# Performance work log

Measured on AMD Instinct MI355X. Metric: run time of the kernel, lower is better.

The kernel has to match this reference:

```python
import jax, jax.numpy as jnp
import numpy as np

N, F, H, O = 3072, 128, 16, 8  # nodes, in_channels, hidden_channels, out_channels


def setup_inputs() -> dict:
    key = jax.random.key(0)
    ks = jax.random.split(key, 8)
    s = 0.01  # xavier gain=0.01 in original init -> small weights
    return {
        "x": jax.random.normal(ks[0], (N, F), dtype=jnp.float32),
        "edge_index": jax.random.randint(ks[1], (2, N * 32), 0, N, dtype=jnp.int64),
        "node_distances": jax.random.uniform(ks[2], (N, N), dtype=jnp.float32),
        "normalization_matrix": jnp.ones((N, N), dtype=jnp.float32),
        # per-feature MLPs fs[f]: Linear(1,H) -> ReLU -> (Dropout p=0) -> Linear(H,O), stacked over F
        "W1": s * jax.random.normal(ks[3], (F, H), dtype=jnp.float32),
        "b1": jnp.zeros((F, H), dtype=jnp.float32),
        "W2": s * jax.random.normal(ks[4], (F, H, O), dtype=jnp.float32),
        "b2": jnp.zeros((F, O), dtype=jnp.float32),
        # rho MLP: Linear(1,H) -> ReLU -> Linear(H,O) (bias=True since is_graph_task=False)
        "rW1": s * jax.random.normal(ks[5], (H,), dtype=jnp.float32),
        "rb1": jnp.zeros((H,), dtype=jnp.float32),
        "rW2": s * jax.random.normal(ks[6], (H, O), dtype=jnp.float32),
        "rb2": jnp.zeros((O,), dtype=jnp.float32),
    }


def reference(x, edge_index, node_distances, normalization_matrix,
              W1, b1, W2, b2, rW1, rb1, rW2, rb2):
    # --- per-feature tiny MLPs, vectorized over the feature axis ---
    # h[n,f,:] = relu(x[n,f] * W1[f] + b1[f])
    h = jax.nn.relu(x[:, :, None] * W1[None, :, :] + b1[None, :, :])  # [N,F,H]
    fx = jnp.einsum('nfh,fho->nfo', h, W2) + b2[None, :, :]           # [N,F,O]
    # sum over features first (commutes with the matmul's F-reduction)
    g = fx.sum(axis=1)                                                 # [N,O]

    # --- rho MLP on normalized pairwise distances ---
    d = node_distances / normalization_matrix                          # [N,N]
    hd = jax.nn.relu(d[:, :, None] * rW1 + rb1)                        # [N,N,H]
    m = jnp.einsum('nmh,ho->nmo', hd, rW2) + rb2                       # [N,N,O]

    # out.T in torch: mf = m_dist_perm @ fx_perm summed over features -> [N,O]
    out = jnp.einsum('nmo,mo->no', m, g)                               # [N,O]
    return out
```

## Files before the change

### kernel.cpp

```cpp
#include <hip/hip_runtime.h>
#include <hip/hip_bf16.h>
#include <math.h>

#define NN 3072
#define FF 128
#define HH 16
#define OO 8

#define OFF_GT   0

#define NPB 4

__global__ __launch_bounds__(128) void gnan_g_kernel(
    const float* __restrict__ x,
    const float* __restrict__ W1,
    const float* __restrict__ b1,
    const float* __restrict__ W2,
    const float* __restrict__ b2,
    float* __restrict__ gT)
{
    const int f  = threadIdx.x;
    const int n0 = blockIdx.x * NPB;

    float xv[NPB];
#pragma unroll
    for (int ni = 0; ni < NPB; ++ni)
        xv[ni] = x[(size_t)(n0 + ni) * FF + f];

    const float4 b2a = *reinterpret_cast<const float4*>(b2 + f * OO);
    const float4 b2b = *reinterpret_cast<const float4*>(b2 + f * OO + 4);

    float acc[NPB][OO];
#pragma unroll
    for (int ni = 0; ni < NPB; ++ni) {
        acc[ni][0] = b2a.x; acc[ni][1] = b2a.y; acc[ni][2] = b2a.z; acc[ni][3] = b2a.w;
        acc[ni][4] = b2b.x; acc[ni][5] = b2b.y; acc[ni][6] = b2b.z; acc[ni][7] = b2b.w;
    }

    for (int h = 0; h < HH; ++h) {
        const float w1h = W1[f * HH + h];
        const float b1h = b1[f * HH + h];
        const float4 wa = *reinterpret_cast<const float4*>(W2 + (size_t)(f * HH + h) * OO);
        const float4 wb = *reinterpret_cast<const float4*>(W2 + (size_t)(f * HH + h) * OO + 4);
#pragma unroll
        for (int ni = 0; ni < NPB; ++ni) {
            const float a = fmaxf(fmaf(xv[ni], w1h, b1h), 0.f);
            acc[ni][0] = fmaf(a, wa.x, acc[ni][0]);
            acc[ni][1] = fmaf(a, wa.y, acc[ni][1]);
            acc[ni][2] = fmaf(a, wa.z, acc[ni][2]);
            acc[ni][3] = fmaf(a, wa.w, acc[ni][3]);
            acc[ni][4] = fmaf(a, wb.x, acc[ni][4]);
            acc[ni][5] = fmaf(a, wb.y, acc[ni][5]);
            acc[ni][6] = fmaf(a, wb.z, acc[ni][6]);
            acc[ni][7] = fmaf(a, wb.w, acc[ni][7]);
        }
    }

    __shared__ float wsum[NPB][2][OO];
    const int lane = threadIdx.x & 63;
    const int wid  = threadIdx.x >> 6;
#pragma unroll
    for (int ni = 0; ni < NPB; ++ni) {
#pragma unroll
        for (int o = 0; o < OO; ++o) {
#pragma unroll
            for (int off = 32; off > 0; off >>= 1)
                acc[ni][o] += __shfl_down(acc[ni][o], off);
        }
        if (lane == 0) {
#pragma unroll
            for (int o = 0; o < OO; ++o) wsum[ni][wid][o] = acc[ni][o];
        }
    }
    __syncthreads();
    if (threadIdx.x < NPB * OO) {
        const int ni = threadIdx.x >> 3, o = threadIdx.x & 7;
        gT[o * NN + (n0 + ni)] = wsum[ni][0][o] + wsum[ni][1][o];
    }
}

__device__ __forceinline__ void accum_one(
    float d, float clo, float chi, const float gk[OO],
    float dg[OO], float sg[OO], float corr[OO],
    const float* KpS, const float (*rowsS)[16], const float* refB)
{
#pragma unroll
    for (int o = 0; o < OO; ++o) sg[o] += gk[o];
    if (d >= clo && d < chi) {
#pragma unroll
        for (int o = 0; o < OO; ++o) dg[o] = fmaf(d, gk[o], dg[o]);
    } else {
        int j = 0;
#pragma unroll
        for (int p = 0; p < HH; ++p) j += (d >= KpS[1 + p]) ? 1 : 0;
#pragma unroll
        for (int o = 0; o < OO; ++o) {
            const float v = fmaf(rowsS[j][o], d, rowsS[j][8 + o]) - refB[o];
            corr[o] = fmaf(v, gk[o], corr[o]);
        }
    }
}

__global__ __launch_bounds__(256) void gnan_main_kernel(
    const float* __restrict__ nd,
    const float* __restrict__ nm,
    const float* __restrict__ gT,
    const float* __restrict__ rW1,
    const float* __restrict__ rb1,
    const float* __restrict__ rW2,
    const float* __restrict__ rb2,
    float* __restrict__ out)
{
    __shared__ float KpS[HH + 2];
    __shared__ float rowsS[HH + 1][16];
    __shared__ float refS[18];

    const int t = threadIdx.x;

    if (t < (HH + 1) * OO + 2) {
        float w[HH], bb[HH], knee[HH];
#pragma unroll
        for (int h = 0; h < HH; ++h) {
            w[h]  = rW1[h];
            bb[h] = rb1[h];
            knee[h] = (w[h] != 0.f) ? (-bb[h] / w[h]) : INFINITY;
        }
        if (t >= (HH + 1) * OO) {
            KpS[(t - (HH + 1) * OO) * (HH + 1)] =
                (t == (HH + 1) * OO) ? -INFINITY : INFINITY;
        } else {
            const int j = t >> 3, o = t & 7;
            if (o == 0 && j < HH) {
                int r = 0;
#pragma unroll
                for (int h2 = 0; h2 < HH; ++h2)
                    r += (knee[h2] < knee[j] || (knee[h2] == knee[j] && h2 < j)) ? 1 : 0;
                KpS[1 + r] = knee[j];
            }
            float cAdd = rb2[o];
#pragma unroll
            for (int h = 0; h < HH; ++h)
                if (w[h] == 0.f) cAdd += fmaxf(bb[h], 0.f) * rW2[h * OO + o];

            float alpha = 0.f, beta = 0.f;
#pragma unroll
            for (int h = 0; h < HH; ++h) {
                int r = 0;
#pragma unroll
                for (int h2 = 0; h2 < HH; ++h2)
                    r += (knee[h2] < knee[h] || (knee[h2] == knee[h] && h2 < h)) ? 1 : 0;
                const bool active = (w[h] > 0.f) ? (r < j)
                                  : (w[h] < 0.f ? (r >= j) : false);
                if (active) {
                    alpha += w[h]  * rW2[h * OO + o];
                    beta  += bb[h] * rW2[h * OO + o];
                }
            }
            const float betaF = beta + cAdd;
            rowsS[j][o]     = alpha;
            rowsS[j][8 + o] = betaF;

            const float d00 = nd[0] / nm[0];
            int j0 = 0;
#pragma unroll
            for (int h = 0; h < HH; ++h) j0 += (d00 >= knee[h]) ? 1 : 0;
            if (j == j0) {
                refS[2 + o]  = alpha;
                refS[10 + o] = betaF;
                if (o == 0) {
                    float clo = -INFINITY, chi = INFINITY;
#pragma unroll
                    for (int h = 0; h < HH; ++h) {
                        if (d00 >= knee[h]) clo = fmaxf(clo, knee[h]);
                        else                chi = fminf(chi, knee[h]);
                    }
                    refS[0] = clo;
                    refS[1] = chi;
                }
            }
        }
    }
    __syncthreads();

    const int wave = t >> 6;
    const int lane = t & 63;
    const int row  = blockIdx.x * 4 + wave;

    const float clo = refS[0];
    const float chi = refS[1];
    const float* refB = &refS[10];

    const float* __restrict__ drow = nd + (size_t)row * NN;
    const float* __restrict__ nrow = nm + (size_t)row * NN;

    float dg[OO], sg[OO], corr[OO];
#pragma unroll
    for (int o = 0; o < OO; ++o) { dg[o] = 0.f; sg[o] = 0.f; corr[o] = 0.f; }

    for (int it = 0; it < NN / 256; ++it) {
        const int m0 = it * 256 + lane * 4;
        const float4 dv = *reinterpret_cast<const float4*>(drow + m0);
        const float4 nv = *reinterpret_cast<const float4*>(nrow + m0);
        float4 gv[OO];
#pragma unroll
        for (int o = 0; o < OO; ++o)
            gv[o] = *reinterpret_cast<const float4*>(&gT[o * NN + m0]);

        {
            float gk[OO];
#pragma unroll
            for (int o = 0; o < OO; ++o) gk[o] = gv[o].x;
            accum_one(__fdividef(dv.x, nv.x), clo, chi, gk, dg, sg, corr, KpS, rowsS, refB);
        }
        {
            float gk[OO];
#pragma unroll
            for (int o = 0; o < OO; ++o) gk[o] = gv[o].y;
            accum_one(__fdividef(dv.y, nv.y), clo, chi, gk, dg, sg, corr, KpS, rowsS, refB);
        }
        {
            float gk[OO];
#pragma unroll
            for (int o = 0; o < OO; ++o) gk[o] = gv[o].z;
            accum_one(__fdividef(dv.z, nv.z), clo, chi, gk, dg, sg, corr, KpS, rowsS, refB);
        }
        {
            float gk[OO];
#pragma unroll
            for (int o = 0; o < OO; ++o) gk[o] = gv[o].w;
            accum_one(__fdividef(dv.w, nv.w), clo, chi, gk, dg, sg, corr, KpS, rowsS, refB);
        }
    }

    float val[OO];
#pragma unroll
    for (int o = 0; o < OO; ++o)
        val[o] = fmaf(refS[2 + o], dg[o], fmaf(refB[o], sg[o], corr[o]));
#pragma unroll
    for (int o = 0; o < OO; ++o) {
#pragma unroll
        for (int off = 32; off > 0; off >>= 1)
            val[o] += __shfl_down(val[o], off);
    }
    if (lane == 0) {
#pragma unroll
        for (int o = 0; o < OO; ++o)
            out[(size_t)row * OO + o] = val[o];
    }
}

extern "C" void kernel_launch(void* const* d_in, const int* in_sizes, int n_in,
                              void* d_out, int out_size, void* d_ws, size_t ws_size,
                              hipStream_t stream) {
    const float* x   = (const float*)d_in[0];
    const float* nd  = (const float*)d_in[2];
    const float* nm  = (const float*)d_in[3];
    const float* W1  = (const float*)d_in[4];
    const float* b1  = (const float*)d_in[5];
    const float* W2  = (const float*)d_in[6];
    const float* b2  = (const float*)d_in[7];
    const float* rW1 = (const float*)d_in[8];
    const float* rb1 = (const float*)d_in[9];
    const float* rW2 = (const float*)d_in[10];
    const float* rb2 = (const float*)d_in[11];
    float* out = (float*)d_out;
    float* wsf = (float*)d_ws;

    gnan_g_kernel<<<NN / NPB, 128, 0, stream>>>(x, W1, b1, W2, b2, wsf + OFF_GT);
    gnan_main_kernel<<<NN / 4, 256, 0, stream>>>(
        nd, nm, wsf + OFF_GT, rW1, rb1, rW2, rb2, out);
}
```

Before: 163.4 us.

## Split main kernel rows across column chunks with atomic accumulation

Each row's reduction over the 3072 columns is split into four column chunks handled by separate blocks, which quadruples the grid. Partial results are combined with atomicAdd into an output buffer that the g kernel now zeroes. The inner loop is fully unrolled and launch bounds request four blocks per CU. The aim is more parallelism and more memory-level parallelism for the bandwidth-bound streaming of two N×N matrices. The cost is atomic traffic, a redundant per-block setup of the rho tables, and nondeterministic summation order.

```diff
diff --git a/kernel.cpp b/kernel.cpp
--- a/kernel.cpp
+++ b/kernel.cpp
@@ -6,6 +6,10 @@
 #define FF 128
 #define HH 16
 #define OO 8
+
+#define SCH  4
+#define MC   (NN / SCH)
+#define WPB  4
 
 #define OFF_GT   0
 
@@ -17,10 +21,17 @@
     const float* __restrict__ b1,
     const float* __restrict__ W2,
     const float* __restrict__ b2,
-    float* __restrict__ gT)
+    float* __restrict__ gT,
+    float* __restrict__ out)
 {
     const int f  = threadIdx.x;
     const int n0 = blockIdx.x * NPB;
+
+    {
+        const int gid = blockIdx.x * 128 + threadIdx.x;
+        if (gid < NN * OO / 4)
+            reinterpret_cast<float4*>(out)[gid] = make_float4(0.f, 0.f, 0.f, 0.f);
+    }
 
     float xv[NPB];
 #pragma unroll
@@ -101,7 +112,7 @@
     }
 }
 
-__global__ __launch_bounds__(256) void gnan_main_kernel(
+__global__ __launch_bounds__(256, 4) void gnan_main_kernel(
     const float* __restrict__ nd,
     const float* __restrict__ nm,
     const float* __restrict__ gT,
@@ -184,27 +195,32 @@
 
     const int wave = t >> 6;
     const int lane = t & 63;
-    const int row  = blockIdx.x * 4 + wave;
+    const int b    = blockIdx.x;
+    const int rg   = b >> 2;
+    const int c    = b & 3;
+    const int row  = rg * WPB + wave;
+    const int mb   = c * MC;
 
     const float clo = refS[0];
     const float chi = refS[1];
     const float* refB = &refS[10];
 
-    const float* __restrict__ drow = nd + (size_t)row * NN;
-    const float* __restrict__ nrow = nm + (size_t)row * NN;
+    const float* __restrict__ drow = nd + (size_t)row * NN + mb;
+    const float* __restrict__ nrow = nm + (size_t)row * NN + mb;
 
     float dg[OO], sg[OO], corr[OO];
 #pragma unroll
     for (int o = 0; o < OO; ++o) { dg[o] = 0.f; sg[o] = 0.f; corr[o] = 0.f; }
 
-    for (int it = 0; it < NN / 256; ++it) {
+#pragma unroll
+    for (int it = 0; it < MC / 256; ++it) {
         const int m0 = it * 256 + lane * 4;
         const float4 dv = *reinterpret_cast<const float4*>(drow + m0);
         const float4 nv = *reinterpret_cast<const float4*>(nrow + m0);
         float4 gv[OO];
 #pragma unroll
         for (int o = 0; o < OO; ++o)
-            gv[o] = *reinterpret_cast<const float4*>(&gT[o * NN + m0]);
+            gv[o] = *reinterpret_cast<const float4*>(&gT[o * NN + mb + m0]);
 
         {
             float gk[OO];
@@ -245,7 +261,7 @@
     if (lane == 0) {
 #pragma unroll
         for (int o = 0; o < OO; ++o)
-            out[(size_t)row * OO + o] = val[o];
+            atomicAdd(out + (size_t)row * OO + o, val[o]);
     }
 }
 
@@ -266,7 +282,8 @@
     float* out = (float*)d_out;
     float* wsf = (float*)d_ws;
 
-    gnan_g_kernel<<<NN / NPB, 128, 0, stream>>>(x, W1, b1, W2, b2, wsf + OFF_GT);
-    gnan_main_kernel<<<NN / 4, 256, 0, stream>>>(
+    gnan_g_kernel<<<NN / NPB, 128, 0, stream>>>(x, W1, b1, W2, b2,
+                                                wsf + OFF_GT, out);
+    gnan_main_kernel<<<(NN / WPB) * SCH, 256, 0, stream>>>(
         nd, nm, wsf + OFF_GT, rW1, rb1, rW2, rb2, out);
 }
```

After: 239.4 us. +46.5%, slower.
